# Performance work log

Measured on AMD Instinct MI355X. Metric: run time of the kernel, lower is better.

Reference implementation:

```python
import jax, jax.numpy as jnp
import numpy as np

N_NODES = 100000
N_EDGES = 1600000
IN_CH = 128
EDGE_CH = 32
HEADS = 4
OUT_CH = 32
NEG_SLOPE = 0.2
EPS = 1e-16  # matches torch_geometric softmax denominator epsilon


def setup_inputs() -> dict:
    key = jax.random.key(0)
    ks = jax.random.split(key, 8)
    x = jax.random.normal(ks[0], (N_NODES, IN_CH), dtype=jnp.float32)
    edge_attr = jax.random.normal(ks[1], (N_EDGES, EDGE_CH), dtype=jnp.float32)
    # glorot-ish scaled params
    Wl = jax.random.normal(ks[2], (HEADS * OUT_CH, IN_CH), dtype=jnp.float32) * (1.0 / np.sqrt(IN_CH))
    We = jax.random.normal(ks[3], (HEADS * OUT_CH, EDGE_CH), dtype=jnp.float32) * (1.0 / np.sqrt(EDGE_CH))
    att_l = jax.random.normal(ks[4], (1, HEADS, OUT_CH), dtype=jnp.float32) * 0.1
    att_r = jax.random.normal(ks[5], (1, HEADS, OUT_CH), dtype=jnp.float32) * 0.1
    att_e = jax.random.normal(ks[6], (1, HEADS, OUT_CH), dtype=jnp.float32) * 0.1
    bias = jnp.zeros((HEADS * OUT_CH,), dtype=jnp.float32)
    edge_index = jax.random.randint(ks[7], (2, N_EDGES), 0, N_NODES, dtype=jnp.int32)
    return {"x": x, "edge_attr": edge_attr, "Wl": Wl, "We": We,
            "att_l": att_l, "att_r": att_r, "att_e": att_e,
            "bias": bias, "edge_index": edge_index}


def reference(x, edge_attr, Wl, We, att_l, att_r, att_e, bias, edge_index):
    N = x.shape[0]
    H, C = att_l.shape[1], att_l.shape[2]
    # shared lin_l == lin_r projection  [N, H, C]
    xl = (x @ Wl.T).reshape(N, H, C)
    alpha_l = (xl * att_l).sum(-1)          # [N, H] source term
    alpha_r = (xl * att_r).sum(-1)          # [N, H] target term
    # edge feature projection            [E, H, C]
    e = (edge_attr @ We.T).reshape(-1, H, C)
    alpha_e = (e * att_e).sum(-1)           # [E, H]
    src, dst = edge_index[0], edge_index[1]
    # per-edge attention logits
    alpha = alpha_l[src] + alpha_r[dst] + alpha_e        # [E, H]
    alpha = jax.nn.leaky_relu(alpha, NEG_SLOPE)
    # segment softmax over incoming edges of each target node
    amax = jax.ops.segment_max(alpha, dst, num_segments=N)   # [N, H]
    ex = jnp.exp(alpha - amax[dst])
    denom = jax.ops.segment_sum(ex, dst, num_segments=N)     # [N, H]
    alpha_n = ex / (denom[dst] + EPS)                        # [E, H]
    # weighted scatter-add aggregation of source features
    msg = xl[src] * alpha_n[:, :, None]                      # [E, H, C]
    out = jax.ops.segment_sum(msg, dst, num_segments=N)      # [N, H, C]
    out = out.reshape(N, H * C) + bias                       # concat heads
    return out
```

## Files before the change

kernel.cpp:

```cpp
#include <hip/hip_runtime.h>
#include <hip/hip_fp16.h>

#define NN 100000
#define NE 1600000
#define NB 391
#define NEG 0.2f

#define OFF_XLB   ((size_t)0)
#define OFF_AL    ((size_t)6400000)
#define OFF_AR    ((size_t)6800000)
#define OFF_WE    ((size_t)7200000)
#define OFF_RECP  ((size_t)7200128)
#define OFF_RECS  ((size_t)10400128)
#define OFF_RANK  ((size_t)12000128)
#define OFF_TMP   OFF_RECP
#define OFF_BSUM  (OFF_RECP + 110000)
#define OFF_DEG   ((size_t)13600128)
#define OFF_ROW   ((size_t)13700128)

__device__ __forceinline__ unsigned short f2bf(float f) {
    unsigned u = __float_as_uint(f);
    u += 0x7fffu + ((u >> 16) & 1u);
    return (unsigned short)(u >> 16);
}
__device__ __forceinline__ float bf2f(unsigned short v) {
    return __uint_as_float((unsigned)v << 16);
}

__global__ void k_prep_zero(const float* __restrict__ We, const float* __restrict__ att_e,
                            float* __restrict__ weT, int* __restrict__ deg) {
    int i = blockIdx.x * 256 + threadIdx.x;
    if (i < NN) deg[i] = 0;
    if (blockIdx.x == 0 && threadIdx.x < 128) {
        int t = threadIdx.x, h = t & 3, k = t >> 2;
        float s = 0.f;
        for (int c = 0; c < 32; ++c)
            s += att_e[h * 32 + c] * We[(size_t)(h * 32 + c) * 32 + k];
        weT[t] = s;
    }
}

__global__ void k_hist(const int* __restrict__ ei, int* __restrict__ deg,
                       int* __restrict__ rank) {
    int e = blockIdx.x * 256 + threadIdx.x;
    rank[e] = atomicAdd(&deg[ei[NE + e]], 1);
}

__global__ __launch_bounds__(256, 2) void k_node(
        const float* __restrict__ x, const float* __restrict__ Wl,
        const float* __restrict__ attl, const float* __restrict__ attr_,
        unsigned short* __restrict__ xlb, float* __restrict__ al, float* __restrict__ ar) {
    __shared__ float wT[128 * 128];
    __shared__ float xT[128 * 32];
    int t = threadIdx.x;
    int og = t & 31, ng = t >> 5;
    int nb = blockIdx.x * 32;

    {
        int o = t & 127, q = t >> 7;
        #pragma unroll
        for (int chunk = 0; chunk < 16; ++chunk) {
            int k0 = chunk * 8 + q * 4;
            float4 w = *(const float4*)&Wl[(size_t)o * 128 + k0];
            wT[(k0 + 0) * 128 + o] = w.x;
            wT[(k0 + 1) * 128 + o] = w.y;
            wT[(k0 + 2) * 128 + o] = w.z;
            wT[(k0 + 3) * 128 + o] = w.w;
        }
    }
    {
        int n = t & 31, q = t >> 5;
        #pragma unroll
        for (int chunk = 0; chunk < 4; ++chunk) {
            int k0 = chunk * 32 + q * 4;
            float4 v = *(const float4*)&x[(size_t)(nb + n) * 128 + k0];
            xT[(k0 + 0) * 32 + n] = v.x;
            xT[(k0 + 1) * 32 + n] = v.y;
            xT[(k0 + 2) * 32 + n] = v.z;
            xT[(k0 + 3) * 32 + n] = v.w;
        }
    }
    float4 attl4 = *(const float4*)&attl[og * 4];
    float4 attr4 = *(const float4*)&attr_[og * 4];
    __syncthreads();

    float4 a0 = make_float4(0,0,0,0), a1 = a0, a2 = a0, a3 = a0;
    #pragma unroll 8
    for (int k = 0; k < 128; ++k) {
        float4 w  = *(const float4*)&wT[k * 128 + og * 4];
        float4 xv = *(const float4*)&xT[k * 32  + ng * 4];
        a0.x += w.x * xv.x; a0.y += w.y * xv.x; a0.z += w.z * xv.x; a0.w += w.w * xv.x;
        a1.x += w.x * xv.y; a1.y += w.y * xv.y; a1.z += w.z * xv.y; a1.w += w.w * xv.y;
        a2.x += w.x * xv.z; a2.y += w.y * xv.z; a2.z += w.z * xv.z; a2.w += w.w * xv.z;
        a3.x += w.x * xv.w; a3.y += w.y * xv.w; a3.z += w.z * xv.w; a3.w += w.w * xv.w;
    }

    float4 accs[4] = {a0, a1, a2, a3};
    #pragma unroll
    for (int j = 0; j < 4; ++j) {
        int node = nb + ng * 4 + j;
        ushort4 pk;
        pk.x = f2bf(accs[j].x); pk.y = f2bf(accs[j].y);
        pk.z = f2bf(accs[j].z); pk.w = f2bf(accs[j].w);
        *(ushort4*)&xlb[(size_t)node * 128 + og * 4] = pk;
        float pl = accs[j].x * attl4.x + accs[j].y * attl4.y +
                   accs[j].z * attl4.z + accs[j].w * attl4.w;
        float pr = accs[j].x * attr4.x + accs[j].y * attr4.y +
                   accs[j].z * attr4.z + accs[j].w * attr4.w;
        #pragma unroll
        for (int off = 1; off <= 4; off <<= 1) {
            pl += __shfl_xor(pl, off);
            pr += __shfl_xor(pr, off);
        }
        if ((og & 7) == 0) {
            al[(size_t)node * 4 + (og >> 3)] = pl;
            ar[(size_t)node * 4 + (og >> 3)] = pr;
        }
    }
}

__global__ void k_scan_block(const int* __restrict__ deg, int* __restrict__ row_tmp,
                             int* __restrict__ bsum) {
    __shared__ int sh[256];
    int t = threadIdx.x, i = blockIdx.x * 256 + t;
    int d = (i < NN) ? deg[i] : 0;
    int v = d;
    sh[t] = v; __syncthreads();
    for (int off = 1; off < 256; off <<= 1) {
        int add = (t >= off) ? sh[t - off] : 0;
        __syncthreads();
        v += add; sh[t] = v; __syncthreads();
    }
    if (i < NN) row_tmp[i] = v - d;
    if (t == 255) bsum[blockIdx.x] = v;
}

__global__ void k_scan_top(int* __restrict__ bsum) {
    __shared__ int sh[512];
    int t = threadIdx.x;
    int d = (t < NB) ? bsum[t] : 0;
    int v = d;
    sh[t] = v; __syncthreads();
    for (int off = 1; off < 512; off <<= 1) {
        int add = (t >= off) ? sh[t - off] : 0;
        __syncthreads();
        v += add; sh[t] = v; __syncthreads();
    }
    if (t < NB) bsum[t] = v - d;
}

__global__ void k_scan_add(const int* __restrict__ row_tmp, const int* __restrict__ bsum,
                           int* __restrict__ row) {
    int i = blockIdx.x * 256 + threadIdx.x;
    if (i < NN) row[i] = row_tmp[i] + bsum[i >> 8];
    if (i == 0) row[NN] = NE;
}

__global__ __launch_bounds__(256) void k_edge(
        const float* __restrict__ eattr, const int* __restrict__ ei,
        const int* __restrict__ rank, const int* __restrict__ row,
        const float* __restrict__ al, const float* __restrict__ ar,
        const float* __restrict__ weT,
        int* __restrict__ rec_src, float2* __restrict__ rec_p) {
    __shared__ float esh[256 * 33];
    int t = threadIdx.x;
    size_t base = (size_t)blockIdx.x * 256 * 32;
    #pragma unroll
    for (int j = 0; j < 8; ++j) {
        int idx = j * 256 + t;
        float4 v = *(const float4*)&eattr[base + (size_t)idx * 4];
        float* d = &esh[(idx >> 3) * 33 + (idx & 7) * 4];
        d[0] = v.x; d[1] = v.y; d[2] = v.z; d[3] = v.w;
    }
    int e = blockIdx.x * 256 + t;
    int src = ei[e], dst = ei[NE + e];
    int rk = rank[e];
    __syncthreads();

    const float* r = &esh[t * 33];
    float a0 = 0.f, a1 = 0.f, a2 = 0.f, a3 = 0.f;
    #pragma unroll
    for (int k = 0; k < 32; ++k) {
        float v = r[k];
        float4 w = *(const float4*)&weT[k * 4];
        a0 += v * w.x; a1 += v * w.y; a2 += v * w.z; a3 += v * w.w;
    }
    float4 ls = *(const float4*)&al[(size_t)src * 4];
    float4 rs = *(const float4*)&ar[(size_t)dst * 4];
    a0 += ls.x + rs.x; a1 += ls.y + rs.y;
    a2 += ls.z + rs.z; a3 += ls.w + rs.w;
    a0 = a0 > 0.f ? a0 : NEG * a0;  a1 = a1 > 0.f ? a1 : NEG * a1;
    a2 = a2 > 0.f ? a2 : NEG * a2;  a3 = a3 > 0.f ? a3 : NEG * a3;
    a0 = __expf(fminf(a0, 60.f)); a1 = __expf(fminf(a1, 60.f));
    a2 = __expf(fminf(a2, 60.f)); a3 = __expf(fminf(a3, 60.f));
    __half2 h01 = __floats2half2_rn(a0, a1);
    __half2 h23 = __floats2half2_rn(a2, a3);
    int slot = row[dst] + rk;
    rec_src[slot] = src;
    float2 p;
    p.x = *reinterpret_cast<float*>(&h01);
    p.y = *reinterpret_cast<float*>(&h23);
    rec_p[slot] = p;
}

__device__ __forceinline__ float pick_p(float2 q, int h) {
    __half2 h01 = *reinterpret_cast<const __half2*>(&q.x);
    __half2 h23 = *reinterpret_cast<const __half2*>(&q.y);
    float2 p01 = __half22float2(h01);
    float2 p23 = __half22float2(h23);
    float lo = (h & 2) ? p23.x : p01.x;
    float hi = (h & 2) ? p23.y : p01.y;
    return (h & 1) ? hi : lo;
}

__global__ __launch_bounds__(128) void k_out(
        const int* __restrict__ row, const int* __restrict__ rec_src,
        const float2* __restrict__ rec_p, const unsigned short* __restrict__ xlb,
        const float* __restrict__ bias, float* __restrict__ out) {
    int n = blockIdx.x;
    int t = threadIdx.x, h = t >> 5;
    int s0 = row[n], s1 = row[n + 1];

    float l0 = 0.f, l1 = 0.f, l2 = 0.f, l3 = 0.f;
    float O0 = 0.f, O1 = 0.f, O2 = 0.f, O3 = 0.f;
    int s = s0;
    for (; s + 4 <= s1; s += 4) {
        int src0 = rec_src[s + 0], src1 = rec_src[s + 1];
        int src2 = rec_src[s + 2], src3 = rec_src[s + 3];
        float2 q0 = rec_p[s + 0], q1 = rec_p[s + 1];
        float2 q2 = rec_p[s + 2], q3 = rec_p[s + 3];
        unsigned short v0 = xlb[(size_t)src0 * 128 + t];
        unsigned short v1 = xlb[(size_t)src1 * 128 + t];
        unsigned short v2 = xlb[(size_t)src2 * 128 + t];
        unsigned short v3 = xlb[(size_t)src3 * 128 + t];
        float p0 = pick_p(q0, h), p1 = pick_p(q1, h);
        float p2 = pick_p(q2, h), p3 = pick_p(q3, h);
        l0 += p0; l1 += p1; l2 += p2; l3 += p3;
        O0 += p0 * bf2f(v0); O1 += p1 * bf2f(v1);
        O2 += p2 * bf2f(v2); O3 += p3 * bf2f(v3);
    }
    for (; s < s1; ++s) {
        int srcn = rec_src[s];
        float p = pick_p(rec_p[s], h);
        l0 += p;
        O0 += p * bf2f(xlb[(size_t)srcn * 128 + t]);
    }
    float l = (l0 + l1) + (l2 + l3);
    float O = (O0 + O1) + (O2 + O3);
    out[(size_t)n * 128 + t] = O / (l + 1e-16f) + bias[t];
}

extern "C" void kernel_launch(void* const* d_in, const int* in_sizes, int n_in,
                              void* d_out, int out_size, void* d_ws, size_t ws_size,
                              hipStream_t stream) {
    const float* x     = (const float*)d_in[0];
    const float* eattr = (const float*)d_in[1];
    const float* Wl    = (const float*)d_in[2];
    const float* We    = (const float*)d_in[3];
    const float* att_l = (const float*)d_in[4];
    const float* att_r = (const float*)d_in[5];
    const float* att_e = (const float*)d_in[6];
    const float* bias  = (const float*)d_in[7];
    const int*   ei    = (const int*)d_in[8];
    float* out = (float*)d_out;

    float* ws = (float*)d_ws;
    unsigned short* xlb = (unsigned short*)(ws + OFF_XLB);
    float*  al      = ws + OFF_AL;
    float*  ar      = ws + OFF_AR;
    float*  weT     = ws + OFF_WE;
    float2* rec_p   = (float2*)(ws + OFF_RECP);
    int*    rec_src = (int*)(ws + OFF_RECS);
    int*    rank    = (int*)(ws + OFF_RANK);
    int*    row_tmp = (int*)(ws + OFF_TMP);
    int*    bsum    = (int*)(ws + OFF_BSUM);
    int*    deg     = (int*)(ws + OFF_DEG);
    int*    rowp    = (int*)(ws + OFF_ROW);

    k_prep_zero<<<NB, 256, 0, stream>>>(We, att_e, weT, deg);
    k_hist<<<NE / 256, 256, 0, stream>>>(ei, deg, rank);
    k_node<<<NN / 32, 256, 0, stream>>>(x, Wl, att_l, att_r, xlb, al, ar);
    k_scan_block<<<NB, 256, 0, stream>>>(deg, row_tmp, bsum);
    k_scan_top<<<1, 512, 0, stream>>>(bsum);
    k_scan_add<<<NB, 256, 0, stream>>>(row_tmp, bsum, rowp);
    k_edge<<<NE / 256, 256, 0, stream>>>(eattr, ei, rank, rowp, al, ar, weT, rec_src, rec_p);
    k_out<<<NN, 128, 0, stream>>>(rowp, rec_src, rec_p, xlb, bias, out);
}
```

Before: 605.1 us.

## Pack edge records into float4, split edges across 8 lanes, halve k_out edge streams

Merges the separate source-index and half-precision weight arrays into a single 16-byte record per edge, so each edge scatter and each aggregation read touches one contiguous record. k_edge now assigns eight lanes per edge to compute the edge-attribute projection with shuffle reductions instead of staging tiles through shared memory. k_out splits the block into two halves that each process alternate edge pairs with 32-bit bf16x2 loads, then combines the halves through shared memory. The record grows from 12 to 16 bytes per edge because of a padding word, and only one lane in eight does the scatter work in k_edge.

```diff
diff --git a/kernel.cpp b/kernel.cpp
--- a/kernel.cpp
+++ b/kernel.cpp
@@ -10,13 +10,12 @@
 #define OFF_AL    ((size_t)6400000)
 #define OFF_AR    ((size_t)6800000)
 #define OFF_WE    ((size_t)7200000)
-#define OFF_RECP  ((size_t)7200128)
-#define OFF_RECS  ((size_t)10400128)
-#define OFF_RANK  ((size_t)12000128)
-#define OFF_TMP   OFF_RECP
-#define OFF_BSUM  (OFF_RECP + 110000)
-#define OFF_DEG   ((size_t)13600128)
-#define OFF_ROW   ((size_t)13700128)
+#define OFF_REC   ((size_t)7200128)
+#define OFF_RANK  ((size_t)13600128)
+#define OFF_TMP   OFF_REC
+#define OFF_BSUM  (OFF_REC + 110000)
+#define OFF_DEG   ((size_t)15200128)
+#define OFF_ROW   ((size_t)15300128)
 
 __device__ __forceinline__ unsigned short f2bf(float f) {
     unsigned u = __float_as_uint(f);
@@ -160,52 +159,51 @@
         const float* __restrict__ eattr, const int* __restrict__ ei,
         const int* __restrict__ rank, const int* __restrict__ row,
         const float* __restrict__ al, const float* __restrict__ ar,
-        const float* __restrict__ weT,
-        int* __restrict__ rec_src, float2* __restrict__ rec_p) {
-    __shared__ float esh[256 * 33];
+        const float* __restrict__ weT, float4* __restrict__ rec) {
     int t = threadIdx.x;
-    size_t base = (size_t)blockIdx.x * 256 * 32;
+    int g = t >> 3, sub = t & 7;
+    int e = blockIdx.x * 32 + g;
+
+    float4 v = *(const float4*)&eattr[(size_t)e * 32 + sub * 4];
+    const float4* wv = (const float4*)weT;
+    float4 w0 = wv[sub * 4 + 0], w1 = wv[sub * 4 + 1];
+    float4 w2 = wv[sub * 4 + 2], w3 = wv[sub * 4 + 3];
+    float a0 = v.x * w0.x + v.y * w1.x + v.z * w2.x + v.w * w3.x;
+    float a1 = v.x * w0.y + v.y * w1.y + v.z * w2.y + v.w * w3.y;
+    float a2 = v.x * w0.z + v.y * w1.z + v.z * w2.z + v.w * w3.z;
+    float a3 = v.x * w0.w + v.y * w1.w + v.z * w2.w + v.w * w3.w;
     #pragma unroll
-    for (int j = 0; j < 8; ++j) {
-        int idx = j * 256 + t;
-        float4 v = *(const float4*)&eattr[base + (size_t)idx * 4];
-        float* d = &esh[(idx >> 3) * 33 + (idx & 7) * 4];
-        d[0] = v.x; d[1] = v.y; d[2] = v.z; d[3] = v.w;
-    }
-    int e = blockIdx.x * 256 + t;
-    int src = ei[e], dst = ei[NE + e];
-    int rk = rank[e];
-    __syncthreads();
-
-    const float* r = &esh[t * 33];
-    float a0 = 0.f, a1 = 0.f, a2 = 0.f, a3 = 0.f;
-    #pragma unroll
-    for (int k = 0; k < 32; ++k) {
-        float v = r[k];
-        float4 w = *(const float4*)&weT[k * 4];
-        a0 += v * w.x; a1 += v * w.y; a2 += v * w.z; a3 += v * w.w;
-    }
-    float4 ls = *(const float4*)&al[(size_t)src * 4];
-    float4 rs = *(const float4*)&ar[(size_t)dst * 4];
-    a0 += ls.x + rs.x; a1 += ls.y + rs.y;
-    a2 += ls.z + rs.z; a3 += ls.w + rs.w;
-    a0 = a0 > 0.f ? a0 : NEG * a0;  a1 = a1 > 0.f ? a1 : NEG * a1;
-    a2 = a2 > 0.f ? a2 : NEG * a2;  a3 = a3 > 0.f ? a3 : NEG * a3;
-    a0 = __expf(fminf(a0, 60.f)); a1 = __expf(fminf(a1, 60.f));
-    a2 = __expf(fminf(a2, 60.f)); a3 = __expf(fminf(a3, 60.f));
-    __half2 h01 = __floats2half2_rn(a0, a1);
-    __half2 h23 = __floats2half2_rn(a2, a3);
-    int slot = row[dst] + rk;
-    rec_src[slot] = src;
-    float2 p;
-    p.x = *reinterpret_cast<float*>(&h01);
-    p.y = *reinterpret_cast<float*>(&h23);
-    rec_p[slot] = p;
-}
-
-__device__ __forceinline__ float pick_p(float2 q, int h) {
-    __half2 h01 = *reinterpret_cast<const __half2*>(&q.x);
-    __half2 h23 = *reinterpret_cast<const __half2*>(&q.y);
+    for (int off = 1; off <= 4; off <<= 1) {
+        a0 += __shfl_xor(a0, off);
+        a1 += __shfl_xor(a1, off);
+        a2 += __shfl_xor(a2, off);
+        a3 += __shfl_xor(a3, off);
+    }
+    if (sub == 0) {
+        int src = ei[e], dst = ei[NE + e];
+        int rk = rank[e];
+        float4 ls = *(const float4*)&al[(size_t)src * 4];
+        float4 rs = *(const float4*)&ar[(size_t)dst * 4];
+        a0 += ls.x + rs.x; a1 += ls.y + rs.y;
+        a2 += ls.z + rs.z; a3 += ls.w + rs.w;
+        a0 = a0 > 0.f ? a0 : NEG * a0;  a1 = a1 > 0.f ? a1 : NEG * a1;
+        a2 = a2 > 0.f ? a2 : NEG * a2;  a3 = a3 > 0.f ? a3 : NEG * a3;
+        a0 = __expf(fminf(a0, 60.f)); a1 = __expf(fminf(a1, 60.f));
+        a2 = __expf(fminf(a2, 60.f)); a3 = __expf(fminf(a3, 60.f));
+        __half2 h01 = __floats2half2_rn(a0, a1);
+        __half2 h23 = __floats2half2_rn(a2, a3);
+        float4 r;
+        r.x = __uint_as_float((unsigned)src);
+        r.y = *reinterpret_cast<float*>(&h01);
+        r.z = *reinterpret_cast<float*>(&h23);
+        r.w = 0.f;
+        rec[row[dst] + rk] = r;
+    }
+}
+
+__device__ __forceinline__ float pick_p(const float4& r, int h) {
+    __half2 h01 = *reinterpret_cast<const __half2*>(&r.y);
+    __half2 h23 = *reinterpret_cast<const __half2*>(&r.z);
     float2 p01 = __half22float2(h01);
     float2 p23 = __half22float2(h23);
     float lo = (h & 2) ? p23.x : p01.x;
@@ -214,40 +212,56 @@
 }
 
 __global__ __launch_bounds__(128) void k_out(
-        const int* __restrict__ row, const int* __restrict__ rec_src,
-        const float2* __restrict__ rec_p, const unsigned short* __restrict__ xlb,
+        const int* __restrict__ row, const float4* __restrict__ rec,
+        const unsigned short* __restrict__ xlb,
         const float* __restrict__ bias, float* __restrict__ out) {
+    __shared__ float shx[2][64], shy[2][64], shl[2][4];
     int n = blockIdx.x;
-    int t = threadIdx.x, h = t >> 5;
+    int t = threadIdx.x;
+    int half = t >> 6, lane = t & 63, h = lane >> 4;
     int s0 = row[n], s1 = row[n + 1];
 
-    float l0 = 0.f, l1 = 0.f, l2 = 0.f, l3 = 0.f;
-    float O0 = 0.f, O1 = 0.f, O2 = 0.f, O3 = 0.f;
+    float l = 0.f, Ox = 0.f, Oy = 0.f;
     int s = s0;
     for (; s + 4 <= s1; s += 4) {
-        int src0 = rec_src[s + 0], src1 = rec_src[s + 1];
-        int src2 = rec_src[s + 2], src3 = rec_src[s + 3];
-        float2 q0 = rec_p[s + 0], q1 = rec_p[s + 1];
-        float2 q2 = rec_p[s + 2], q3 = rec_p[s + 3];
-        unsigned short v0 = xlb[(size_t)src0 * 128 + t];
-        unsigned short v1 = xlb[(size_t)src1 * 128 + t];
-        unsigned short v2 = xlb[(size_t)src2 * 128 + t];
-        unsigned short v3 = xlb[(size_t)src3 * 128 + t];
-        float p0 = pick_p(q0, h), p1 = pick_p(q1, h);
-        float p2 = pick_p(q2, h), p3 = pick_p(q3, h);
-        l0 += p0; l1 += p1; l2 += p2; l3 += p3;
-        O0 += p0 * bf2f(v0); O1 += p1 * bf2f(v1);
-        O2 += p2 * bf2f(v2); O3 += p3 * bf2f(v3);
-    }
-    for (; s < s1; ++s) {
-        int srcn = rec_src[s];
-        float p = pick_p(rec_p[s], h);
-        l0 += p;
-        O0 += p * bf2f(xlb[(size_t)srcn * 128 + t]);
-    }
-    float l = (l0 + l1) + (l2 + l3);
-    float O = (O0 + O1) + (O2 + O3);
-    out[(size_t)n * 128 + t] = O / (l + 1e-16f) + bias[t];
+        int sa = s + half * 2;
+        float4 r0 = rec[sa], r1 = rec[sa + 1];
+        int src0 = (int)__float_as_uint(r0.x);
+        int src1 = (int)__float_as_uint(r1.x);
+        unsigned v0 = *(const unsigned*)&xlb[(size_t)src0 * 128 + lane * 2];
+        unsigned v1 = *(const unsigned*)&xlb[(size_t)src1 * 128 + lane * 2];
+        float p0 = pick_p(r0, h), p1 = pick_p(r1, h);
+        l += p0 + p1;
+        Ox += p0 * bf2f((unsigned short)(v0 & 0xffffu))
+            + p1 * bf2f((unsigned short)(v1 & 0xffffu));
+        Oy += p0 * bf2f((unsigned short)(v0 >> 16))
+            + p1 * bf2f((unsigned short)(v1 >> 16));
+    }
+    if (half == 0) {
+        for (; s < s1; ++s) {
+            float4 r = rec[s];
+            int srcn = (int)__float_as_uint(r.x);
+            unsigned v = *(const unsigned*)&xlb[(size_t)srcn * 128 + lane * 2];
+            float p = pick_p(r, h);
+            l += p;
+            Ox += p * bf2f((unsigned short)(v & 0xffffu));
+            Oy += p * bf2f((unsigned short)(v >> 16));
+        }
+    }
+    shx[half][lane] = Ox;
+    shy[half][lane] = Oy;
+    if ((lane & 15) == 0) shl[half][h] = l;
+    __syncthreads();
+    if (half == 0) {
+        float X = shx[0][lane] + shx[1][lane];
+        float Y = shy[0][lane] + shy[1][lane];
+        float inv = 1.f / (shl[0][h] + shl[1][h] + 1e-16f);
+        float2 b = *(const float2*)&bias[lane * 2];
+        float2 o;
+        o.x = X * inv + b.x;
+        o.y = Y * inv + b.y;
+        *(float2*)&out[(size_t)n * 128 + lane * 2] = o;
+    }
 }
 
 extern "C" void kernel_launch(void* const* d_in, const int* in_sizes, int n_in,
@@ -269,8 +283,7 @@
     float*  al      = ws + OFF_AL;
     float*  ar      = ws + OFF_AR;
     float*  weT     = ws + OFF_WE;
-    float2* rec_p   = (float2*)(ws + OFF_RECP);
-    int*    rec_src = (int*)(ws + OFF_RECS);
+    float4* rec     = (float4*)(ws + OFF_REC);
     int*    rank    = (int*)(ws + OFF_RANK);
     int*    row_tmp = (int*)(ws + OFF_TMP);
     int*    bsum    = (int*)(ws + OFF_BSUM);
@@ -283,6 +296,6 @@
     k_scan_block<<<NB, 256, 0, stream>>>(deg, row_tmp, bsum);
     k_scan_top<<<1, 512, 0, stream>>>(bsum);
     k_scan_add<<<NB, 256, 0, stream>>>(row_tmp, bsum, rowp);
-    k_edge<<<NE / 256, 256, 0, stream>>>(eattr, ei, rank, rowp, al, ar, weT, rec_src, rec_p);
-    k_out<<<NN, 128, 0, stream>>>(rowp, rec_src, rec_p, xlb, bias, out);
-}
+    k_edge<<<NE / 32, 256, 0, stream>>>(eattr, ei, rank, rowp, al, ar, weT, rec);
+    k_out<<<NN, 128, 0, stream>>>(rowp, rec, xlb, bias, out);
+}
```

Result: slower. 621.7 us (+2.7%).
